# Performance work log

Hardware: AMD Instinct MI355X
Metric: run time of the kernel (lower is better)

The kernel has to match this reference:

```python
import jax, jax.numpy as jnp
import numpy as np

N = 100000      # nodes
E = 1600000     # edges (avg degree 16)
FEAT, HID, OUT = 128, 64, 40
P_DROP = 0.5


def setup_inputs() -> dict:
    key = jax.random.key(0)
    ks = jax.random.split(key, 7)
    x = jax.random.normal(ks[0], (N, FEAT), dtype=jnp.float32)
    edge_index = jax.random.randint(ks[1], (2, E), 0, N, dtype=jnp.int32)
    W1 = jax.random.normal(ks[2], (FEAT, HID), dtype=jnp.float32) / np.float32(np.sqrt(FEAT))
    b1 = jnp.zeros((HID,), jnp.float32)
    W2 = jax.random.normal(ks[3], (HID, OUT), dtype=jnp.float32) / np.float32(np.sqrt(HID))
    b2 = jnp.zeros((OUT,), jnp.float32)
    # scaled inverted-dropout mask: values in {0, 1/(1-p)}
    keep = jax.random.bernoulli(ks[4], 1.0 - P_DROP, (N, HID))
    drop_mask = keep.astype(jnp.float32) / np.float32(1.0 - P_DROP)
    return {"x": x, "edge_index": edge_index, "W1": W1, "b1": b1,
            "W2": W2, "b2": b2, "drop_mask": drop_mask}


def _gcn_conv(x, W, b, src, dst):
    """PyG GCNConv: h = xW; add self-loops; sym-normalized scatter-add; +b."""
    h = x @ W                                   # [N, D_out]
    ones = jnp.ones((src.shape[0],), h.dtype)
    deg = jax.ops.segment_sum(ones, dst, num_segments=N) + 1.0  # +1 self-loop
    dinv = jax.lax.rsqrt(deg)                   # deg > 0 due to self-loops
    norm = dinv[src] * dinv[dst]                # [E]
    msg = h[src] * norm[:, None]                # gather + scale
    agg = jax.ops.segment_sum(msg, dst, num_segments=N)
    agg = agg + h * (dinv * dinv)[:, None]      # self-loop contribution
    return agg + b


def reference(x, edge_index, W1, b1, W2, b2, drop_mask):
    src, dst = edge_index[0], edge_index[1]
    h = _gcn_conv(x, W1, b1, src, dst)
    h = jax.nn.relu(h)
    h = h * drop_mask                           # F.dropout (pre-drawn mask)
    out = _gcn_conv(h, W2, b2, src, dst)
    return out
```

## Files before the change

### kernel.cpp

```cpp
#include <hip/hip_runtime.h>
#include <hip/hip_fp16.h>

#define NN     100000
#define NE     1600000
#define FEAT   128
#define HID    64
#define OUTD   40
#define BNODES 32
#define NSB    ((NN + 255) / 256)
#define NBAGG  (NSB * 8)
#define CAP    5120
#define CCHUNK 4096
#define WSCALE 262144.0f
#define WINV   (1.0f / 262144.0f)

typedef _Float16 half8 __attribute__((ext_vector_type(8)));
typedef float    f32x4 __attribute__((ext_vector_type(4)));

__global__ __launch_bounds__(256) void k_pairs(const int* __restrict__ src,
                                               const int* __restrict__ dst,
                                               int* __restrict__ bfill,
                                               int* __restrict__ pairs) {
    __shared__ int bcnt[NSB];
    __shared__ int gb[NSB];
    int t = threadIdx.x;
    for (int i = t; i < NSB; i += 256) bcnt[i] = 0;
    __syncthreads();
    const int4* d4p = (const int4*)dst;
    const int4* s4p = (const int4*)src;
    int q0 = blockIdx.x * (CCHUNK / 4);
    int4 dv[4], sv[4];
    int off[16];
    #pragma unroll
    for (int i = 0; i < 4; ++i) {
        int q = q0 + i * 256 + t;
        if (q < NE / 4) {
            dv[i] = d4p[q];
            sv[i] = s4p[q];
            off[i*4+0] = atomicAdd(&bcnt[dv[i].x >> 8], 1);
            off[i*4+1] = atomicAdd(&bcnt[dv[i].y >> 8], 1);
            off[i*4+2] = atomicAdd(&bcnt[dv[i].z >> 8], 1);
            off[i*4+3] = atomicAdd(&bcnt[dv[i].w >> 8], 1);
        } else dv[i].x = -1;
    }
    __syncthreads();
    for (int i = t; i < NSB; i += 256) {
        int c = bcnt[i];
        gb[i] = c ? (i * CAP + atomicAdd(&bfill[i], c)) : 0;
    }
    __syncthreads();
    #pragma unroll
    for (int i = 0; i < 4; ++i) {
        if (dv[i].x >= 0) {
            pairs[gb[dv[i].x >> 8] + off[i*4+0]] = (sv[i].x << 8) | (dv[i].x & 255);
            pairs[gb[dv[i].y >> 8] + off[i*4+1]] = (sv[i].y << 8) | (dv[i].y & 255);
            pairs[gb[dv[i].z >> 8] + off[i*4+2]] = (sv[i].z << 8) | (dv[i].z & 255);
            pairs[gb[dv[i].w >> 8] + off[i*4+3]] = (sv[i].w << 8) | (dv[i].w & 255);
        }
    }
}

__global__ __launch_bounds__(256) void k_csr(const int* __restrict__ pairs,
                                             const int* __restrict__ bfill,
                                             int* __restrict__ sb_beg,
                                             int* __restrict__ sb_cnt,
                                             int* __restrict__ csr,
                                             float* __restrict__ dinv) {
    __shared__ int hist[2048];
    __shared__ int exs[2048];
    __shared__ int nd[256];
    __shared__ int part[256];
    __shared__ int poff[9];
    __shared__ int sstart[8];
    __shared__ int dtot[8];
    int b = blockIdx.x, t = threadIdx.x;
    #pragma unroll
    for (int k = 0; k < 8; ++k) hist[t * 8 + k] = 0;
    nd[t] = 0;
    __syncthreads();
    int base = b * CAP, count = bfill[b];
    for (int i = t; i < count; i += 256) {
        int p = pairs[base + i];
        int key = (((p & 255) >> 5) << 8) | ((p >> 17) & 255);
        atomicAdd(&hist[key], 1);
        atomicAdd(&nd[p & 255], 1);
    }
    __syncthreads();
    {
        int node = (b << 8) + t;
        if (node < NN) dinv[node] = rsqrtf((float)nd[t] + 1.0f);
    }
    int loc[8], s0 = 0;
    #pragma unroll
    for (int k = 0; k < 8; ++k) { loc[k] = s0; s0 += hist[t * 8 + k]; }
    part[t] = s0;
    __syncthreads();
    for (int off = 1; off < 256; off <<= 1) {
        int u = (t >= off) ? part[t - off] : 0;
        __syncthreads();
        part[t] += u;
        __syncthreads();
    }
    int pex = part[t] - s0;
    #pragma unroll
    for (int k = 0; k < 8; ++k) exs[t * 8 + k] = pex + loc[k];
    __syncthreads();
    if (t < 8) {
        sstart[t] = exs[t * 256];
        int end = (t == 7) ? count : exs[(t + 1) * 256];
        dtot[t] = end - sstart[t];
    }
    __syncthreads();
    if (t == 0) {
        poff[0] = 0;
        for (int d = 0; d < 8; ++d) poff[d + 1] = poff[d] + ((dtot[d] + 31) & ~31);
    }
    __syncthreads();
    #pragma unroll
    for (int k = 0; k < 8; ++k) {
        int key = t * 8 + k;
        int d = key >> 8;
        exs[key] = poff[d] + (exs[key] - sstart[d]);
        hist[key] = 0;
    }
    __syncthreads();
    for (int i = t; i < count; i += 256) {
        int p = pairs[base + i];
        int key = (((p & 255) >> 5) << 8) | ((p >> 17) & 255);
        int pos = exs[key] + atomicAdd(&hist[key], 1);
        csr[base + pos] = ((p >> 8) << 7) | (p & 31);
    }
    for (int d = 0; d < 8; ++d) {
        int padded = (dtot[d] + 31) & ~31;
        for (int i = dtot[d] + t; i < padded; i += 256)
            csr[base + poff[d] + i] = (NN << 7);
    }
    if (t < 8) {
        sb_beg[b * 8 + t] = base + poff[t];
        sb_cnt[b * 8 + t] = (dtot[t] + 31) & ~31;
    }
}

__global__ __launch_bounds__(256) void k_maskbits(const float* __restrict__ mask,
                                                  unsigned long long* __restrict__ mb) {
    int node = blockIdx.x * 4 + (threadIdx.x >> 6);
    if (node >= NN) return;
    int l = threadIdx.x & 63;
    float m = mask[(size_t)node * HID + l];
    unsigned long long bits = __ballot(m != 0.f);
    if (l == 0) mb[node] = bits;
}

__global__ __launch_bounds__(256) void k_wprep(const float* __restrict__ W1,
                                               const float* __restrict__ W2,
                                               _Float16* __restrict__ w1f,
                                               _Float16* __restrict__ w2f,
                                               __half* __restrict__ h1s,
                                               __half* __restrict__ hhs) {
    int t = threadIdx.x;
    for (int it = t; it < 16 * 64; it += 256) {
        int f = it >> 6, l = it & 63;
        int kk = f >> 2, n = f & 3;
        int krow = kk * 32 + (l >> 4) * 8;
        int col  = n * 16 + (l & 15);
        #pragma unroll
        for (int i = 0; i < 8; ++i)
            w1f[it * 8 + i] = (_Float16)W1[(krow + i) * HID + col];
    }
    for (int it = t; it < 6 * 64; it += 256) {
        int f = it >> 6, l = it & 63;
        int kk = f / 3, n = f - kk * 3;
        int krow = kk * 32 + (l >> 4) * 8;
        int col  = n * 16 + (l & 15);
        #pragma unroll
        for (int i = 0; i < 8; ++i)
            w2f[it * 8 + i] = (col < OUTD) ? (_Float16)W2[(krow + i) * OUTD + col]
                                           : (_Float16)0.f;
    }
    if (t < HID) {
        h1s[(size_t)NN * HID + t] = __float2half(0.f);
        hhs[(size_t)NN * HID + t] = __float2half(0.f);
    }
}

__global__ __launch_bounds__(256) void k_mgemm1(const float* __restrict__ x,
                                                const _Float16* __restrict__ w1f,
                                                const float* __restrict__ dinv,
                                                __half* __restrict__ h1s) {
    int wid = (blockIdx.x * 256 + threadIdx.x) >> 6;
    int l = threadIdx.x & 63;
    if (wid >= NN / 16) return;
    half8 bf[4][4];
    #pragma unroll
    for (int kk = 0; kk < 4; ++kk)
        #pragma unroll
        for (int n = 0; n < 4; ++n)
            bf[kk][n] = ((const half8*)w1f)[(kk * 4 + n) * 64 + l];
    f32x4 acc[4] = {};
    int arow = wid * 16 + (l & 15);
    const float* xp = x + (size_t)arow * FEAT + (l >> 4) * 8;
    #pragma unroll
    for (int kk = 0; kk < 4; ++kk) {
        float4 u0 = *(const float4*)(xp + kk * 32);
        float4 u1 = *(const float4*)(xp + kk * 32 + 4);
        half8 af;
        af[0] = (_Float16)u0.x; af[1] = (_Float16)u0.y;
        af[2] = (_Float16)u0.z; af[3] = (_Float16)u0.w;
        af[4] = (_Float16)u1.x; af[5] = (_Float16)u1.y;
        af[6] = (_Float16)u1.z; af[7] = (_Float16)u1.w;
        #pragma unroll
        for (int n = 0; n < 4; ++n)
            acc[n] = __builtin_amdgcn_mfma_f32_16x16x32_f16(af, bf[kk][n], acc[n], 0, 0, 0);
    }
    int orow = wid * 16 + (l >> 4) * 4;
    int ocol = l & 15;
    float dv[4];
    #pragma unroll
    for (int r = 0; r < 4; ++r) dv[r] = dinv[orow + r];
    #pragma unroll
    for (int n = 0; n < 4; ++n)
        #pragma unroll
        for (int r = 0; r < 4; ++r)
            h1s[(size_t)(orow + r) * HID + n * 16 + ocol] = __float2half(acc[n][r] * dv[r]);
}

template<int MODE>
__global__ __launch_bounds__(256) void k_bagg(const int* __restrict__ csr,
                                              const int* __restrict__ sb_beg,
                                              const int* __restrict__ sb_cnt,
                                              const float* __restrict__ dinv,
                                              const __half* __restrict__ feat,
                                              const float* __restrict__ b1,
                                              const unsigned long long* __restrict__ maskbits,
                                              __half* __restrict__ outp,
                                              const _Float16* __restrict__ w2f,
                                              const float* __restrict__ b2,
                                              float* __restrict__ outf) {
    __shared__ int acc[BNODES * HID];
    int t = threadIdx.x, wv = t >> 6, l = t & 63;
    int bb = blockIdx.x;
    int4* a4 = (int4*)acc;
    for (int i = t; i < BNODES * HID / 4; i += 256) a4[i] = make_int4(0, 0, 0, 0);
    __syncthreads();
    int base  = sb_beg[bb];
    int count = sb_cnt[bb];
    int node0 = (bb >> 3) * 256 + (bb & 7) * 32;
    const char* fb = (const char*)feat + ((size_t)l * 2);
    for (int j = wv * 16; j < count; j += 64) {
        int e[16];
        #pragma unroll
        for (int i = 0; i < 16; ++i) e[i] = csr[base + j + i];
        float a[16];
        #pragma unroll
        for (int i = 0; i < 16; ++i)
            a[i] = __half2float(*(const __half*)(fb + (unsigned)(e[i] & ~127)));
        #pragma unroll
        for (int i = 0; i < 16; ++i)
            atomicAdd(&acc[((e[i] & 31) << 6) + l], (int)(a[i] * WSCALE));
    }
    __syncthreads();
    if constexpr (MODE == 0) {
        for (int n = wv; n < BNODES; n += 4) {
            int node = node0 + n;
            if (node >= NN) break;
            float di = dinv[node];
            float selfv = __half2float(feat[(size_t)node * HID + l]);
            float vv = ((float)acc[(n << 6) + l] * WINV + selfv) * di;
            vv += b1[l];
            vv = vv > 0.f ? vv : 0.f;
            unsigned long long mb = maskbits[node];
            vv = ((mb >> l) & 1ull) ? vv * 2.0f * di : 0.0f;
            outp[(size_t)node * HID + l] = __float2half(vv);
        }
    } else {
        __shared__ _Float16 aggf[BNODES][72];
        for (int n = wv; n < BNODES; n += 4) {
            int node = node0 + n;
            float v = 0.f;
            if (node < NN) {
                float di = dinv[node];
                float selfv = __half2float(feat[(size_t)node * HID + l]);
                v = ((float)acc[(n << 6) + l] * WINV + selfv) * di;
            }
            aggf[n][l] = (_Float16)v;
        }
        __syncthreads();
        if (wv < 2) {
            half8 bf[2][3];
            #pragma unroll
            for (int kk = 0; kk < 2; ++kk)
                #pragma unroll
                for (int n = 0; n < 3; ++n)
                    bf[kk][n] = ((const half8*)w2f)[(kk * 3 + n) * 64 + l];
            int lrow = wv * 16 + (l & 15);
            int k0 = (l >> 4) * 8;
            f32x4 o[3] = {};
            #pragma unroll
            for (int kk = 0; kk < 2; ++kk) {
                half8 af = *(const half8*)&aggf[lrow][kk * 32 + k0];
                #pragma unroll
                for (int n = 0; n < 3; ++n)
                    o[n] = __builtin_amdgcn_mfma_f32_16x16x32_f16(af, bf[kk][n], o[n], 0, 0, 0);
            }
            int orow = node0 + wv * 16 + (l >> 4) * 4;
            int ocol = l & 15;
            #pragma unroll
            for (int n = 0; n < 3; ++n) {
                int col = n * 16 + ocol;
                if (col < OUTD) {
                    float bbias = b2[col];
                    #pragma unroll
                    for (int r = 0; r < 4; ++r) {
                        int row = orow + r;
                        if (row < NN)
                            outf[(size_t)row * OUTD + col] = o[n][r] + bbias;
                    }
                }
            }
        }
    }
}

extern "C" void kernel_launch(void* const* d_in, const int* in_sizes, int n_in,
                              void* d_out, int out_size, void* d_ws, size_t ws_size,
                              hipStream_t stream) {
    const float* x    = (const float*)d_in[0];
    const int*   ei   = (const int*)d_in[1];
    const int*   src  = ei;
    const int*   dst  = ei + NE;
    const float* W1   = (const float*)d_in[2];
    const float* b1   = (const float*)d_in[3];
    const float* W2   = (const float*)d_in[4];
    const float* b2   = (const float*)d_in[5];
    const float* mask = (const float*)d_in[6];
    float* out = (float*)d_out;

    char* ws = (char*)d_ws;
    int*      bfill  = (int*)ws;           ws += (size_t)NSB * 4;
    int*      sb_beg = (int*)ws;           ws += (size_t)NBAGG * 4;
    int*      sb_cnt = (int*)ws;           ws += (size_t)NBAGG * 4;
    float*    dinv   = (float*)ws;         ws += (size_t)NN * 4;
    unsigned long long* maskb = (unsigned long long*)ws; ws += (size_t)NN * 8;
    _Float16* w1f    = (_Float16*)ws;      ws += 16 * 64 * 8 * 2;
    _Float16* w2f    = (_Float16*)ws;      ws += 6 * 64 * 8 * 2;
    int*      csr    = (int*)ws;           ws += (size_t)NSB * CAP * 4;
    __half*   h1s    = (__half*)ws;        ws += (size_t)(NN + 1) * HID * 2;
    __half*   hhs    = (__half*)ws;        ws += (size_t)(NN + 1) * HID * 2;
    int*      pairs  = (int*)hhs;

    hipMemsetAsync(bfill, 0, (size_t)NSB * 4, stream);

    k_pairs   <<<(NE + CCHUNK - 1) / CCHUNK, 256, 0, stream>>>(src, dst, bfill, pairs);
    k_csr     <<<NSB, 256, 0, stream>>>(pairs, bfill, sb_beg, sb_cnt, csr, dinv);
    k_maskbits<<<(NN + 3) / 4, 256, 0, stream>>>(mask, maskb);
    k_wprep   <<<1, 256, 0, stream>>>(W1, W2, w1f, w2f, h1s, hhs);

    k_mgemm1  <<<(NN / 16 + 3) / 4, 256, 0, stream>>>(x, w1f, dinv, h1s);
    k_bagg<0> <<<NBAGG, 256, 0, stream>>>(csr, sb_beg, sb_cnt, dinv, h1s, b1, maskb,
                                          hhs, nullptr, nullptr, nullptr);
    k_bagg<1> <<<NBAGG, 256, 0, stream>>>(csr, sb_beg, sb_cnt, dinv, hhs, nullptr, nullptr,
                                          nullptr, w2f, b2, out);
}
```

Measured before the change: 170.8 us.

## Store intermediate features as fixed-point int16 and drop mask bitpacking kernel

Intermediate node features are now stored as scaled int16 fixed-point values instead of fp16. The gather loop can then feed the integer shared-memory atomics directly, with no half-to-float conversion and scale multiply per edge. The separate mask-ballot kernel is removed, and the float dropout mask is read directly in the first aggregation epilogue. The risk is precision: int16 with scales of 4096 and 2048 may overflow or lose resolution for large or small values, and the mask read moves 64 floats per node into the epilogue.

```diff
diff --git a/kernel.cpp b/kernel.cpp
--- a/kernel.cpp
+++ b/kernel.cpp
@@ -11,8 +11,10 @@
 #define NBAGG  (NSB * 8)
 #define CAP    5120
 #define CCHUNK 4096
-#define WSCALE 262144.0f
-#define WINV   (1.0f / 262144.0f)
+#define S1     4096.0f
+#define S1INV  (1.0f / 4096.0f)
+#define S2     2048.0f
+#define S2INV  (1.0f / 2048.0f)
 
 typedef _Float16 half8 __attribute__((ext_vector_type(8)));
 typedef float    f32x4 __attribute__((ext_vector_type(4)));
@@ -141,22 +143,12 @@
     }
 }
 
-__global__ __launch_bounds__(256) void k_maskbits(const float* __restrict__ mask,
-                                                  unsigned long long* __restrict__ mb) {
-    int node = blockIdx.x * 4 + (threadIdx.x >> 6);
-    if (node >= NN) return;
-    int l = threadIdx.x & 63;
-    float m = mask[(size_t)node * HID + l];
-    unsigned long long bits = __ballot(m != 0.f);
-    if (l == 0) mb[node] = bits;
-}
-
 __global__ __launch_bounds__(256) void k_wprep(const float* __restrict__ W1,
                                                const float* __restrict__ W2,
                                                _Float16* __restrict__ w1f,
                                                _Float16* __restrict__ w2f,
-                                               __half* __restrict__ h1s,
-                                               __half* __restrict__ hhs) {
+                                               short* __restrict__ h1s,
+                                               short* __restrict__ hhs) {
     int t = threadIdx.x;
     for (int it = t; it < 16 * 64; it += 256) {
         int f = it >> 6, l = it & 63;
@@ -178,15 +170,15 @@
                                            : (_Float16)0.f;
     }
     if (t < HID) {
-        h1s[(size_t)NN * HID + t] = __float2half(0.f);
-        hhs[(size_t)NN * HID + t] = __float2half(0.f);
+        h1s[(size_t)NN * HID + t] = 0;
+        hhs[(size_t)NN * HID + t] = 0;
     }
 }
 
 __global__ __launch_bounds__(256) void k_mgemm1(const float* __restrict__ x,
                                                 const _Float16* __restrict__ w1f,
                                                 const float* __restrict__ dinv,
-                                                __half* __restrict__ h1s) {
+                                                short* __restrict__ h1s) {
     int wid = (blockIdx.x * 256 + threadIdx.x) >> 6;
     int l = threadIdx.x & 63;
     if (wid >= NN / 16) return;
@@ -216,12 +208,13 @@
     int ocol = l & 15;
     float dv[4];
     #pragma unroll
-    for (int r = 0; r < 4; ++r) dv[r] = dinv[orow + r];
+    for (int r = 0; r < 4; ++r) dv[r] = dinv[orow + r] * S1;
     #pragma unroll
     for (int n = 0; n < 4; ++n)
         #pragma unroll
         for (int r = 0; r < 4; ++r)
-            h1s[(size_t)(orow + r) * HID + n * 16 + ocol] = __float2half(acc[n][r] * dv[r]);
+            h1s[(size_t)(orow + r) * HID + n * 16 + ocol] =
+                (short)__float2int_rn(acc[n][r] * dv[r]);
 }
 
 template<int MODE>
@@ -229,10 +222,10 @@
                                               const int* __restrict__ sb_beg,
                                               const int* __restrict__ sb_cnt,
                                               const float* __restrict__ dinv,
-                                              const __half* __restrict__ feat,
+                                              const short* __restrict__ feat,
                                               const float* __restrict__ b1,
-                                              const unsigned long long* __restrict__ maskbits,
-                                              __half* __restrict__ outp,
+                                              const float* __restrict__ mask,
+                                              short* __restrict__ outp,
                                               const _Float16* __restrict__ w2f,
                                               const float* __restrict__ b2,
                                               float* __restrict__ outf) {
@@ -250,13 +243,13 @@
         int e[16];
         #pragma unroll
         for (int i = 0; i < 16; ++i) e[i] = csr[base + j + i];
-        float a[16];
+        int v[16];
         #pragma unroll
         for (int i = 0; i < 16; ++i)
-            a[i] = __half2float(*(const __half*)(fb + (unsigned)(e[i] & ~127)));
+            v[i] = (int)*(const short*)(fb + (unsigned)(e[i] & ~127));
         #pragma unroll
         for (int i = 0; i < 16; ++i)
-            atomicAdd(&acc[((e[i] & 31) << 6) + l], (int)(a[i] * WSCALE));
+            atomicAdd(&acc[((e[i] & 31) << 6) + l], v[i]);
     }
     __syncthreads();
     if constexpr (MODE == 0) {
@@ -264,13 +257,12 @@
             int node = node0 + n;
             if (node >= NN) break;
             float di = dinv[node];
-            float selfv = __half2float(feat[(size_t)node * HID + l]);
-            float vv = ((float)acc[(n << 6) + l] * WINV + selfv) * di;
+            int selfv = (int)feat[(size_t)node * HID + l];
+            float vv = (float)(acc[(n << 6) + l] + selfv) * S1INV * di;
             vv += b1[l];
             vv = vv > 0.f ? vv : 0.f;
-            unsigned long long mb = maskbits[node];
-            vv = ((mb >> l) & 1ull) ? vv * 2.0f * di : 0.0f;
-            outp[(size_t)node * HID + l] = __float2half(vv);
+            vv *= mask[(size_t)node * HID + l] * di;
+            outp[(size_t)node * HID + l] = (short)__float2int_rn(vv * S2);
         }
     } else {
         __shared__ _Float16 aggf[BNODES][72];
@@ -279,8 +271,8 @@
             float v = 0.f;
             if (node < NN) {
                 float di = dinv[node];
-                float selfv = __half2float(feat[(size_t)node * HID + l]);
-                v = ((float)acc[(n << 6) + l] * WINV + selfv) * di;
+                int selfv = (int)feat[(size_t)node * HID + l];
+                v = (float)(acc[(n << 6) + l] + selfv) * S2INV * di;
             }
             aggf[n][l] = (_Float16)v;
         }
@@ -340,24 +332,22 @@
     int*      sb_beg = (int*)ws;           ws += (size_t)NBAGG * 4;
     int*      sb_cnt = (int*)ws;           ws += (size_t)NBAGG * 4;
     float*    dinv   = (float*)ws;         ws += (size_t)NN * 4;
-    unsigned long long* maskb = (unsigned long long*)ws; ws += (size_t)NN * 8;
     _Float16* w1f    = (_Float16*)ws;      ws += 16 * 64 * 8 * 2;
     _Float16* w2f    = (_Float16*)ws;      ws += 6 * 64 * 8 * 2;
     int*      csr    = (int*)ws;           ws += (size_t)NSB * CAP * 4;
-    __half*   h1s    = (__half*)ws;        ws += (size_t)(NN + 1) * HID * 2;
-    __half*   hhs    = (__half*)ws;        ws += (size_t)(NN + 1) * HID * 2;
+    short*    h1s    = (short*)ws;         ws += (size_t)(NN + 1) * HID * 2;
+    short*    hhs    = (short*)ws;         ws += (size_t)(NN + 1) * HID * 2;
     int*      pairs  = (int*)hhs;
 
     hipMemsetAsync(bfill, 0, (size_t)NSB * 4, stream);
 
-    k_pairs   <<<(NE + CCHUNK - 1) / CCHUNK, 256, 0, stream>>>(src, dst, bfill, pairs);
-    k_csr     <<<NSB, 256, 0, stream>>>(pairs, bfill, sb_beg, sb_cnt, csr, dinv);
-    k_maskbits<<<(NN + 3) / 4, 256, 0, stream>>>(mask, maskb);
-    k_wprep   <<<1, 256, 0, stream>>>(W1, W2, w1f, w2f, h1s, hhs);
-
-    k_mgemm1  <<<(NN / 16 + 3) / 4, 256, 0, stream>>>(x, w1f, dinv, h1s);
-    k_bagg<0> <<<NBAGG, 256, 0, stream>>>(csr, sb_beg, sb_cnt, dinv, h1s, b1, maskb,
-                                          hhs, nullptr, nullptr, nullptr);
-    k_bagg<1> <<<NBAGG, 256, 0, stream>>>(csr, sb_beg, sb_cnt, dinv, hhs, nullptr, nullptr,
-                                          nullptr, w2f, b2, out);
-}
+    k_pairs <<<(NE + CCHUNK - 1) / CCHUNK, 256, 0, stream>>>(src, dst, bfill, pairs);
+    k_csr   <<<NSB, 256, 0, stream>>>(pairs, bfill, sb_beg, sb_cnt, csr, dinv);
+    k_wprep <<<1, 256, 0, stream>>>(W1, W2, w1f, w2f, h1s, hhs);
+
+    k_mgemm1<<<(NN / 16 + 3) / 4, 256, 0, stream>>>(x, w1f, dinv, h1s);
+    k_bagg<0><<<NBAGG, 256, 0, stream>>>(csr, sb_beg, sb_cnt, dinv, h1s, b1, mask,
+                                         hhs, nullptr, nullptr, nullptr);
+    k_bagg<1><<<NBAGG, 256, 0, stream>>>(csr, sb_beg, sb_cnt, dinv, hhs, nullptr, nullptr,
+                                         nullptr, w2f, b2, out);
+}
```

Result: faster. 164.8 us, median of 2 (-3.5%).
